# Performance work log

Hardware: AMD Instinct MI355X
Metric: run time of the kernel (lower is better)

The kernel has to match this reference:

```python
import jax, jax.numpy as jnp
import numpy as np

NUM_LEVELS = 16
BASE_RES = 16
MAX_RES = 2048
F_PER_LEVEL = 2
MAX_TABLE = 524288  # 2**19
N_POINTS = 1048576
# geometric resolution schedule, identical to the torch module
RESOLUTIONS = [int(BASE_RES * (MAX_RES / BASE_RES) ** (l / (NUM_LEVELS - 1))) for l in range(NUM_LEVELS)]
TABLE_SIZES = [min(r ** 3, MAX_TABLE) for r in RESOLUTIONS]


def setup_inputs() -> dict:
    key = jax.random.key(0)
    k0, k1, k2, k3 = jax.random.split(key, 4)
    coords = jax.random.uniform(k0, (N_POINTS, 3), minval=-1.0, maxval=1.0, dtype=jnp.float32)
    # hash tables init U(-1e-4, 1e-4); all padded to MAX_TABLE rows (levels with
    # smaller dense tables simply never index past TABLE_SIZES[l])
    tables = jax.random.uniform(k1, (NUM_LEVELS, MAX_TABLE, F_PER_LEVEL), minval=-1e-4, maxval=1e-4, dtype=jnp.float32)
    d_in = NUM_LEVELS * F_PER_LEVEL  # 32
    W1 = jax.random.normal(k2, (d_in, 128), dtype=jnp.float32) * (2.0 / (d_in + 128)) ** 0.5
    b1 = jnp.zeros((128,), dtype=jnp.float32)
    W2 = jax.random.normal(k3, (128, 64), dtype=jnp.float32) * (2.0 / (128 + 64)) ** 0.5
    b2 = jnp.zeros((64,), dtype=jnp.float32)
    return {"coords": coords, "tables": tables, "W1": W1, "b1": b1, "W2": W2, "b2": b2}


def _hash_gather(coords, tables):
    # coords: [N, 3] in [-1, 1] -> normalized to [0, 1]
    c = (coords + 1.0) * 0.5
    feats = []
    for l in range(NUM_LEVELS):
        R = RESOLUTIONS[l]
        T = TABLE_SIZES[l]
        d = jnp.clip(jnp.floor(c * R).astype(jnp.int32), 0, R - 1).astype(jnp.uint32)  # [N, 3]
        # (x*R^2 + y*R + z) % T in uint32. Wraparound mod 2^32 only occurs at the
        # finest levels where T = 2^19 divides 2^32, so the result stays exact.
        idx = (d[:, 0] * jnp.uint32(R * R) + d[:, 1] * jnp.uint32(R) + d[:, 2]) % jnp.uint32(T)
        feats.append(tables[l][idx.astype(jnp.int32)])  # [N, F_PER_LEVEL]
    return jnp.concatenate(feats, axis=-1)  # [N, 32], level-major


def reference(coords, tables, W1, b1, W2, b2):
    x = _hash_gather(coords, tables)              # [N, 32]
    h = jax.nn.relu(x @ W1 + b1)                  # [N, 128]
    return h @ W2 + b2                            # [N, 64]
```

## Files before the change

### kernel.cpp

```cpp
#include <hip/hip_runtime.h>
#include <stdint.h>


typedef __attribute__((ext_vector_type(8))) __bf16 bf16x8;
typedef __attribute__((ext_vector_type(4))) float  f32x4;
typedef __attribute__((ext_vector_type(2))) float  f32x2;

#define NPTS   1048576
#define NTILES 65536

__device__ const unsigned kRES[16] = {16u,22u,30u,42u,58u,80u,111u,153u,
                                      212u,294u,406u,561u,776u,1072u,1482u,2048u};

__device__ __forceinline__ unsigned pack_bf16(float x, float y) {
  __bf16 a = (__bf16)x, b = (__bf16)y;
  unsigned short ua, ub;
  __builtin_memcpy(&ua, &a, 2);
  __builtin_memcpy(&ub, &b, 2);
  return (unsigned)ua | ((unsigned)ub << 16);
}

__global__ __launch_bounds__(256) void tconv_prep_kernel(
    const float* __restrict__ tables,
    const float* __restrict__ W1, const float* __restrict__ W2,
    unsigned* __restrict__ tb2, short* __restrict__ w1p, short* __restrict__ w2p)
{
  if (blockIdx.x < 8192) {
    int e0 = (blockIdx.x * 256 + threadIdx.x) * 4;
#pragma unroll
    for (int i = 0; i < 4; ++i) {
      int e = e0 + i;
      f32x2 f = *(const f32x2*)(tables + (size_t)e * 2);
      tb2[e] = pack_bf16(f.x, f.y);
    }
    return;
  }
  int tid = (blockIdx.x - 8192) * 256 + threadIdx.x;
  int l = tid & 63;
  int g = l >> 4;
  int c = l & 15;
  if (tid < 512) {
    int t = tid >> 6;
    bf16x8 v;
#pragma unroll
    for (int j = 0; j < 8; ++j)
      v[j] = (__bf16)W1[(8*g + j)*128 + 16*t + c];
    *(bf16x8*)(w1p + (size_t)(t*64 + l)*8) = v;
  } else if (tid < 1536) {
    int e = (tid - 512) >> 6;
    int mt = e >> 2, ks = e & 3;
    bf16x8 v;
#pragma unroll
    for (int j = 0; j < 8; ++j)
      v[j] = (__bf16)W2[(32*ks + 16*(j>>2) + 4*g + (j&3))*64 + 16*mt + c];
    *(bf16x8*)(w2p + (size_t)(e*64 + l)*8) = v;
  }
}

__global__ __launch_bounds__(256) void gather_kernel(
    const float* __restrict__ coords, const unsigned* __restrict__ tb2,
    unsigned* __restrict__ xw)
{
  const int xcd = blockIdx.x & 7;
  const int j   = blockIdx.x >> 3;
  int lv, chunk;
  if (j < 1408) {
    int ghi = xcd * 1408 + j;
    lv = 5 + (ghi >> 10);
    chunk = ghi & 1023;
  } else {
    int gei = xcd * 640 + (j - 1408);
    lv = gei >> 10;
    chunk = gei & 1023;
  }

  const unsigned R = kRES[lv];
  const float fR = (float)R;
  const unsigned RR = R * R;
  const unsigned Rm1 = R - 1u;
  const unsigned M = (lv >= 6) ? 0x7FFFFu : 0xFFFFFFFFu;
  const unsigned* tb = tb2 + ((size_t)lv << 19);
  unsigned* xp = xw + ((size_t)lv << 20);

  int p0 = chunk * 1024 + threadIdx.x;
#pragma unroll
  for (int i = 0; i < 4; ++i) {
    int p = p0 + (i << 8);
    float u0 = (coords[3*p+0] + 1.0f) * 0.5f;
    float u1 = (coords[3*p+1] + 1.0f) * 0.5f;
    float u2 = (coords[3*p+2] + 1.0f) * 0.5f;
    unsigned d0 = (unsigned)(int)(u0 * fR); if (d0 > Rm1) d0 = Rm1;
    unsigned d1 = (unsigned)(int)(u1 * fR); if (d1 > Rm1) d1 = Rm1;
    unsigned d2 = (unsigned)(int)(u2 * fR); if (d2 > Rm1) d2 = Rm1;
    unsigned idx = (d0*RR + d1*R + d2) & M;
    xp[p] = tb[idx];
  }
}

__global__ __launch_bounds__(256, 4) void mlp_kernel(
    const unsigned* __restrict__ xw,
    const float* __restrict__ b1, const float* __restrict__ b2,
    const short* __restrict__ w1p, const short* __restrict__ w2p,
    float* __restrict__ out)
{
  const int l = threadIdx.x & 63;
  const int g = l >> 4;
  const int c = l & 15;
  const int w = threadIdx.x >> 6;

  __shared__ float obuf[4][16][68];

  bf16x8 w1f[8];
#pragma unroll
  for (int t = 0; t < 8; ++t)
    w1f[t] = *(const bf16x8*)(w1p + (size_t)(t*64 + l)*8);

  const int base = blockIdx.x * 4 + w;

  unsigned gx[4][4];
#pragma unroll
  for (int it = 0; it < 4; ++it) {
    int p = (base + it*16384)*16 + c;
#pragma unroll
    for (int q = 0; q < 4; ++q)
      gx[it][q] = xw[((size_t)(4*g + q) << 20) + p];
  }

#pragma unroll
  for (int it = 0; it < 4; ++it) {
    union { bf16x8 v; unsigned u[4]; } X;
#pragma unroll
    for (int q = 0; q < 4; ++q) X.u[q] = gx[it][q];
    bf16x8 xf = X.v;

    f32x4 h[8];
#pragma unroll
    for (int t = 0; t < 8; ++t) {
      h[t] = *(const f32x4*)(b1 + 16*t + 4*g);
      h[t] = __builtin_amdgcn_mfma_f32_16x16x32_bf16(w1f[t], xf, h[t], 0, 0, 0);
    }

    f32x4 o[4];
#pragma unroll
    for (int mt = 0; mt < 4; ++mt)
      o[mt] = *(const f32x4*)(b2 + 16*mt + 4*g);
#pragma unroll
    for (int ks = 0; ks < 4; ++ks) {
      bf16x8 bp;
#pragma unroll
      for (int j = 0; j < 8; ++j) {
        float v = h[2*ks + (j>>2)][j & 3];
        v = fmaxf(v, 0.0f);
        bp[j] = (__bf16)v;
      }
#pragma unroll
      for (int mt = 0; mt < 4; ++mt) {
        bf16x8 w2f = *(const bf16x8*)(w2p + (size_t)((mt*4 + ks)*64 + l)*8);
        o[mt] = __builtin_amdgcn_mfma_f32_16x16x32_bf16(w2f, bp, o[mt], 0, 0, 0);
      }
    }

    float (*ob)[68] = obuf[w];
#pragma unroll
    for (int mt = 0; mt < 4; ++mt)
      *(f32x4*)&ob[c][16*mt + 4*g] = o[mt];
    asm volatile("s_waitcnt lgkmcnt(0)" ::: "memory");
    f32x4 v[4];
#pragma unroll
    for (int s = 0; s < 4; ++s)
      v[s] = *(const f32x4*)&ob[4*s + g][4*c];
    asm volatile("" ::: "memory");
    float* op = out + (size_t)(base + it*16384) * 1024;
#pragma unroll
    for (int s = 0; s < 4; ++s)
      *(f32x4*)(op + (4*s + g)*64 + 4*c) = v[s];

    if (it < 3) asm volatile("s_waitcnt lgkmcnt(0)" ::: "memory");
  }
}

__global__ void prep_kernel(const float* __restrict__ W1, const float* __restrict__ W2,
                            short* __restrict__ w1p, short* __restrict__ w2p) {
  int tid = blockIdx.x * blockDim.x + threadIdx.x;
  int l = tid & 63;
  int g = l >> 4;
  int c = l & 15;
  if (tid < 512) {
    int t = tid >> 6;
    bf16x8 v;
#pragma unroll
    for (int j = 0; j < 8; ++j)
      v[j] = (__bf16)W1[(8*g + j)*128 + 16*t + c];
    *(bf16x8*)(w1p + (size_t)(t*64 + l)*8) = v;
  } else if (tid < 1536) {
    int e = (tid - 512) >> 6;
    int mt = e >> 2, ks = e & 3;
    bf16x8 v;
#pragma unroll
    for (int j = 0; j < 8; ++j)
      v[j] = (__bf16)W2[(32*ks + 16*(j>>2) + 4*g + (j&3))*64 + 16*mt + c];
    *(bf16x8*)(w2p + (size_t)(e*64 + l)*8) = v;
  }
}

__global__ __launch_bounds__(256, 3) void hashgrid_mlp_kernel(
    const float* __restrict__ coords, const float* __restrict__ tables,
    const float* __restrict__ b1, const float* __restrict__ b2,
    const short* __restrict__ w1p, const short* __restrict__ w2p,
    float* __restrict__ out, int stride)
{
  const int l = threadIdx.x & 63;
  const int g = l >> 4;
  const int c = l & 15;

  unsigned Rq[4], RRq[4], Mq[4]; float fRq[4];
#pragma unroll
  for (int q = 0; q < 4; ++q) {
    int lv = 4*g + q;
    unsigned R = kRES[lv];
    Rq[q] = R; RRq[q] = R*R; fRq[q] = (float)R;
    Mq[q] = (lv >= 6) ? 0x7FFFFu : 0xFFFFFFFFu;
  }
  const float* tb = tables + ((size_t)g << 22);

  bf16x8 w1f[8];
#pragma unroll
  for (int t = 0; t < 8; ++t)
    w1f[t] = *(const bf16x8*)(w1p + (size_t)(t*64 + l)*8);

  f32x2 gx[4];
  auto prefetch = [&](int tile) {
    int p = tile*16 + c;
    float u0 = (coords[3*p+0] + 1.0f) * 0.5f;
    float u1 = (coords[3*p+1] + 1.0f) * 0.5f;
    float u2 = (coords[3*p+2] + 1.0f) * 0.5f;
#pragma unroll
    for (int q = 0; q < 4; ++q) {
      unsigned Rm1 = Rq[q] - 1u;
      unsigned d0 = (unsigned)(int)(u0 * fRq[q]); if (d0 > Rm1) d0 = Rm1;
      unsigned d1 = (unsigned)(int)(u1 * fRq[q]); if (d1 > Rm1) d1 = Rm1;
      unsigned d2 = (unsigned)(int)(u2 * fRq[q]); if (d2 > Rm1) d2 = Rm1;
      unsigned idx = (d0*RRq[q] + d1*Rq[q] + d2) & Mq[q];
      gx[q] = *(const f32x2*)(tb + ((size_t)q << 20) + (size_t)idx*2u);
    }
  };

  int tile = blockIdx.x * 4 + (threadIdx.x >> 6);
  prefetch(tile);
  while (true) {
    bf16x8 xf;
#pragma unroll
    for (int q = 0; q < 4; ++q) {
      xf[2*q]   = (__bf16)gx[q].x;
      xf[2*q+1] = (__bf16)gx[q].y;
    }
    int cur = tile;
    tile += stride;
    if (tile < NTILES) prefetch(tile);

    f32x4 h[8];
#pragma unroll
    for (int t = 0; t < 8; ++t) {
      h[t] = *(const f32x4*)(b1 + 16*t + 4*g);
      h[t] = __builtin_amdgcn_mfma_f32_16x16x32_bf16(w1f[t], xf, h[t], 0, 0, 0);
    }

    f32x4 o[4];
#pragma unroll
    for (int mt = 0; mt < 4; ++mt)
      o[mt] = *(const f32x4*)(b2 + 16*mt + 4*g);
#pragma unroll
    for (int ks = 0; ks < 4; ++ks) {
      bf16x8 bp;
#pragma unroll
      for (int j = 0; j < 8; ++j) {
        float v = h[2*ks + (j>>2)][j & 3];
        v = fmaxf(v, 0.0f);
        bp[j] = (__bf16)v;
      }
#pragma unroll
      for (int mt = 0; mt < 4; ++mt) {
        bf16x8 w2f = *(const bf16x8*)(w2p + (size_t)((mt*4 + ks)*64 + l)*8);
        o[mt] = __builtin_amdgcn_mfma_f32_16x16x32_bf16(w2f, bp, o[mt], 0, 0, 0);
      }
    }

    float* op = out + (size_t)(cur*16 + c)*64 + 4*g;
#pragma unroll
    for (int mt = 0; mt < 4; ++mt)
      *(f32x4*)(op + 16*mt) = o[mt];

    if (tile >= NTILES) break;
  }
}

extern "C" void kernel_launch(void* const* d_in, const int* in_sizes, int n_in,
                              void* d_out, int out_size, void* d_ws, size_t ws_size,
                              hipStream_t stream) {
  const float* coords = (const float*)d_in[0];
  const float* tables = (const float*)d_in[1];
  const float* W1     = (const float*)d_in[2];
  const float* b1     = (const float*)d_in[3];
  const float* W2     = (const float*)d_in[4];
  const float* b2     = (const float*)d_in[5];
  float* out = (float*)d_out;

  short* w1p = (short*)d_ws;
  short* w2p = w1p + 4096;

  const size_t XW_OFF  = 32*1024;
  const size_t XW_SZ   = (size_t)NPTS * 16 * 4;
  const size_t TB2_SZ  = (size_t)16 * 524288 * 4;
  const size_t need = XW_OFF + XW_SZ + TB2_SZ;

  if (ws_size >= need) {
    unsigned* xw  = (unsigned*)((char*)d_ws + XW_OFF);
    unsigned* tb2 = (unsigned*)((char*)d_ws + XW_OFF + XW_SZ);
    tconv_prep_kernel<<<8198, 256, 0, stream>>>(tables, W1, W2, tb2, w1p, w2p);
    gather_kernel<<<16384, 256, 0, stream>>>(coords, tb2, xw);
    mlp_kernel<<<4096, 256, 0, stream>>>(xw, b1, b2, w1p, w2p, out);
  } else {
    prep_kernel<<<6, 256, 0, stream>>>(W1, W2, w1p, w2p);
    const int blocks = 2048;
    hashgrid_mlp_kernel<<<blocks, 256, 0, stream>>>(coords, tables, b1, b2,
                                                    w1p, w2p, out, blocks*4);
  }
}
```

Measured before the change: 188.3 us.

## Fuse hash gather and MLP into one kernel with LDS transpose

Replaces the separate gather kernel, which wrote a 64 MB bf16 feature buffer to global memory, and the MLP kernel that read it back, with one fused kernel. Each thread computes all 16 level indices for one point, gathers the packed table entries into registers, and stages them in shared memory so the MFMA fragments can be read per 16-point tile. This removes the intermediate global write and read plus one launch. The cost is that the level-interleaved, XCD-aware gather schedule is lost, so the random table accesses from all 16 levels now compete for L2 at the same time, and the kernel uses more registers and LDS.

```diff
diff --git a/kernel.cpp b/kernel.cpp
--- a/kernel.cpp
+++ b/kernel.cpp
@@ -8,9 +8,6 @@
 
 #define NPTS   1048576
 #define NTILES 65536
-
-__device__ const unsigned kRES[16] = {16u,22u,30u,42u,58u,80u,111u,153u,
-                                      212u,294u,406u,561u,776u,1072u,1482u,2048u};
 
 __device__ __forceinline__ unsigned pack_bf16(float x, float y) {
   __bf16 a = (__bf16)x, b = (__bf16)y;
@@ -57,48 +54,8 @@
   }
 }
 
-__global__ __launch_bounds__(256) void gather_kernel(
+__global__ __launch_bounds__(256) void fused_kernel(
     const float* __restrict__ coords, const unsigned* __restrict__ tb2,
-    unsigned* __restrict__ xw)
-{
-  const int xcd = blockIdx.x & 7;
-  const int j   = blockIdx.x >> 3;
-  int lv, chunk;
-  if (j < 1408) {
-    int ghi = xcd * 1408 + j;
-    lv = 5 + (ghi >> 10);
-    chunk = ghi & 1023;
-  } else {
-    int gei = xcd * 640 + (j - 1408);
-    lv = gei >> 10;
-    chunk = gei & 1023;
-  }
-
-  const unsigned R = kRES[lv];
-  const float fR = (float)R;
-  const unsigned RR = R * R;
-  const unsigned Rm1 = R - 1u;
-  const unsigned M = (lv >= 6) ? 0x7FFFFu : 0xFFFFFFFFu;
-  const unsigned* tb = tb2 + ((size_t)lv << 19);
-  unsigned* xp = xw + ((size_t)lv << 20);
-
-  int p0 = chunk * 1024 + threadIdx.x;
-#pragma unroll
-  for (int i = 0; i < 4; ++i) {
-    int p = p0 + (i << 8);
-    float u0 = (coords[3*p+0] + 1.0f) * 0.5f;
-    float u1 = (coords[3*p+1] + 1.0f) * 0.5f;
-    float u2 = (coords[3*p+2] + 1.0f) * 0.5f;
-    unsigned d0 = (unsigned)(int)(u0 * fR); if (d0 > Rm1) d0 = Rm1;
-    unsigned d1 = (unsigned)(int)(u1 * fR); if (d1 > Rm1) d1 = Rm1;
-    unsigned d2 = (unsigned)(int)(u2 * fR); if (d2 > Rm1) d2 = Rm1;
-    unsigned idx = (d0*RR + d1*R + d2) & M;
-    xp[p] = tb[idx];
-  }
-}
-
-__global__ __launch_bounds__(256, 4) void mlp_kernel(
-    const unsigned* __restrict__ xw,
     const float* __restrict__ b1, const float* __restrict__ b2,
     const short* __restrict__ w1p, const short* __restrict__ w2p,
     float* __restrict__ out)
@@ -108,36 +65,56 @@
   const int c = l & 15;
   const int w = threadIdx.x >> 6;
 
+  __shared__ unsigned xbuf[256][20];
   __shared__ float obuf[4][16][68];
+
+  constexpr unsigned Rt[16] = {16u,22u,30u,42u,58u,80u,111u,153u,
+                               212u,294u,406u,561u,776u,1072u,1482u,2048u};
 
   bf16x8 w1f[8];
 #pragma unroll
   for (int t = 0; t < 8; ++t)
     w1f[t] = *(const bf16x8*)(w1p + (size_t)(t*64 + l)*8);
 
-  const int base = blockIdx.x * 4 + w;
-
-  unsigned gx[4][4];
-#pragma unroll
-  for (int it = 0; it < 4; ++it) {
-    int p = (base + it*16384)*16 + c;
-#pragma unroll
-    for (int q = 0; q < 4; ++q)
-      gx[it][q] = xw[((size_t)(4*g + q) << 20) + p];
-  }
-
-#pragma unroll
-  for (int it = 0; it < 4; ++it) {
-    union { bf16x8 v; unsigned u[4]; } X;
-#pragma unroll
-    for (int q = 0; q < 4; ++q) X.u[q] = gx[it][q];
+  const int ptl = w*64 + l;
+  const int p   = blockIdx.x*256 + ptl;
+  const float u0 = (coords[3*p+0] + 1.0f) * 0.5f;
+  const float u1 = (coords[3*p+1] + 1.0f) * 0.5f;
+  const float u2 = (coords[3*p+2] + 1.0f) * 0.5f;
+
+  unsigned idx[16];
+#pragma unroll
+  for (int lv = 0; lv < 16; ++lv) {
+    const unsigned R = Rt[lv];
+    const float fR = (float)R;
+    const unsigned Rm1 = R - 1u;
+    const unsigned M = (lv >= 6) ? 0x7FFFFu : 0xFFFFFFFFu;
+    unsigned d0 = (unsigned)(int)(u0 * fR); if (d0 > Rm1) d0 = Rm1;
+    unsigned d1 = (unsigned)(int)(u1 * fR); if (d1 > Rm1) d1 = Rm1;
+    unsigned d2 = (unsigned)(int)(u2 * fR); if (d2 > Rm1) d2 = Rm1;
+    idx[lv] = (d0*(R*R) + d1*R + d2) & M;
+  }
+  unsigned val[16];
+#pragma unroll
+  for (int lv = 0; lv < 16; ++lv)
+    val[lv] = tb2[((size_t)lv << 19) + idx[lv]];
+#pragma unroll
+  for (int lv = 0; lv < 16; ++lv)
+    xbuf[ptl][lv] = val[lv];
+  asm volatile("s_waitcnt lgkmcnt(0)" ::: "memory");
+  __builtin_amdgcn_sched_barrier(0);
+
+#pragma unroll
+  for (int t = 0; t < 4; ++t) {
+    union { bf16x8 v; f32x4 f; } X;
+    X.f = *(const f32x4*)&xbuf[w*64 + t*16 + c][4*g];
     bf16x8 xf = X.v;
 
     f32x4 h[8];
 #pragma unroll
-    for (int t = 0; t < 8; ++t) {
-      h[t] = *(const f32x4*)(b1 + 16*t + 4*g);
-      h[t] = __builtin_amdgcn_mfma_f32_16x16x32_bf16(w1f[t], xf, h[t], 0, 0, 0);
+    for (int tt = 0; tt < 8; ++tt) {
+      h[tt] = *(const f32x4*)(b1 + 16*tt + 4*g);
+      h[tt] = __builtin_amdgcn_mfma_f32_16x16x32_bf16(w1f[tt], xf, h[tt], 0, 0, 0);
     }
 
     f32x4 o[4];
@@ -170,12 +147,11 @@
     for (int s = 0; s < 4; ++s)
       v[s] = *(const f32x4*)&ob[4*s + g][4*c];
     asm volatile("" ::: "memory");
-    float* op = out + (size_t)(base + it*16384) * 1024;
+    float* op = out + (size_t)(blockIdx.x*16 + w*4 + t) * 1024;
 #pragma unroll
     for (int s = 0; s < 4; ++s)
       *(f32x4*)(op + (4*s + g)*64 + 4*c) = v[s];
-
-    if (it < 3) asm volatile("s_waitcnt lgkmcnt(0)" ::: "memory");
+    if (t < 3) asm volatile("s_waitcnt lgkmcnt(0)" ::: "memory");
   }
 }
 
@@ -202,6 +178,9 @@
     *(bf16x8*)(w2p + (size_t)(e*64 + l)*8) = v;
   }
 }
+
+__device__ const unsigned kRES[16] = {16u,22u,30u,42u,58u,80u,111u,153u,
+                                      212u,294u,406u,561u,776u,1072u,1482u,2048u};
 
 __global__ __launch_bounds__(256, 3) void hashgrid_mlp_kernel(
     const float* __restrict__ coords, const float* __restrict__ tables,
@@ -308,17 +287,14 @@
   short* w1p = (short*)d_ws;
   short* w2p = w1p + 4096;
 
-  const size_t XW_OFF  = 32*1024;
-  const size_t XW_SZ   = (size_t)NPTS * 16 * 4;
+  const size_t TB2_OFF = 32*1024;
   const size_t TB2_SZ  = (size_t)16 * 524288 * 4;
-  const size_t need = XW_OFF + XW_SZ + TB2_SZ;
+  const size_t need = TB2_OFF + TB2_SZ;
 
   if (ws_size >= need) {
-    unsigned* xw  = (unsigned*)((char*)d_ws + XW_OFF);
-    unsigned* tb2 = (unsigned*)((char*)d_ws + XW_OFF + XW_SZ);
+    unsigned* tb2 = (unsigned*)((char*)d_ws + TB2_OFF);
     tconv_prep_kernel<<<8198, 256, 0, stream>>>(tables, W1, W2, tb2, w1p, w2p);
-    gather_kernel<<<16384, 256, 0, stream>>>(coords, tb2, xw);
-    mlp_kernel<<<4096, 256, 0, stream>>>(xw, b1, b2, w1p, w2p, out);
+    fused_kernel<<<4096, 256, 0, stream>>>(coords, tb2, b1, b2, w1p, w2p, out);
   } else {
     prep_kernel<<<6, 256, 0, stream>>>(W1, W2, w1p, w2p);
     const int blocks = 2048;
```

Result: slower. 287.6 us (+52.7%).

## Fuse coarse hash levels into one gather pass and halve MLP per-block work

Applied to the files above, without the earlier changes.

The gather kernel's blocks for the five coarse levels (0-4) now process all five levels for each point, so coordinates are read once instead of five times. This cuts the gather grid from 16384 to 12288 blocks, and the resolution table becomes a compile-time constant. The MLP kernel now handles two tiles per wave instead of four and launches twice as many blocks, trading register prefetch depth for more parallelism. Coarse-level blocks do more serial work, which may unbalance the load against the fine-level blocks.

```diff
diff --git a/kernel.cpp b/kernel.cpp
--- a/kernel.cpp
+++ b/kernel.cpp
@@ -8,9 +8,6 @@
 
 #define NPTS   1048576
 #define NTILES 65536
-
-__device__ const unsigned kRES[16] = {16u,22u,30u,42u,58u,80u,111u,153u,
-                                      212u,294u,406u,561u,776u,1072u,1482u,2048u};
 
 __device__ __forceinline__ unsigned pack_bf16(float x, float y) {
   __bf16 a = (__bf16)x, b = (__bf16)y;
@@ -61,39 +58,57 @@
     const float* __restrict__ coords, const unsigned* __restrict__ tb2,
     unsigned* __restrict__ xw)
 {
+  constexpr unsigned Rt[16] = {16u,22u,30u,42u,58u,80u,111u,153u,
+                               212u,294u,406u,561u,776u,1072u,1482u,2048u};
   const int xcd = blockIdx.x & 7;
   const int j   = blockIdx.x >> 3;
-  int lv, chunk;
+
   if (j < 1408) {
     int ghi = xcd * 1408 + j;
-    lv = 5 + (ghi >> 10);
-    chunk = ghi & 1023;
+    int lv = 5 + (ghi >> 10);
+    int chunk = ghi & 1023;
+
+    const unsigned R = Rt[lv];
+    const float fR = (float)R;
+    const unsigned RR = R * R;
+    const unsigned Rm1 = R - 1u;
+    const unsigned M = (lv >= 6) ? 0x7FFFFu : 0xFFFFFFFFu;
+    const unsigned* tb = tb2 + ((size_t)lv << 19);
+    unsigned* xp = xw + ((size_t)lv << 20);
+
+    int p0 = chunk * 1024 + threadIdx.x;
+#pragma unroll
+    for (int i = 0; i < 4; ++i) {
+      int p = p0 + (i << 8);
+      float u0 = (coords[3*p+0] + 1.0f) * 0.5f;
+      float u1 = (coords[3*p+1] + 1.0f) * 0.5f;
+      float u2 = (coords[3*p+2] + 1.0f) * 0.5f;
+      unsigned d0 = (unsigned)(int)(u0 * fR); if (d0 > Rm1) d0 = Rm1;
+      unsigned d1 = (unsigned)(int)(u1 * fR); if (d1 > Rm1) d1 = Rm1;
+      unsigned d2 = (unsigned)(int)(u2 * fR); if (d2 > Rm1) d2 = Rm1;
+      unsigned idx = (d0*RR + d1*R + d2) & M;
+      xp[p] = tb[idx];
+    }
   } else {
-    int gei = xcd * 640 + (j - 1408);
-    lv = gei >> 10;
-    chunk = gei & 1023;
-  }
-
-  const unsigned R = kRES[lv];
-  const float fR = (float)R;
-  const unsigned RR = R * R;
-  const unsigned Rm1 = R - 1u;
-  const unsigned M = (lv >= 6) ? 0x7FFFFu : 0xFFFFFFFFu;
-  const unsigned* tb = tb2 + ((size_t)lv << 19);
-  unsigned* xp = xw + ((size_t)lv << 20);
-
-  int p0 = chunk * 1024 + threadIdx.x;
-#pragma unroll
-  for (int i = 0; i < 4; ++i) {
-    int p = p0 + (i << 8);
-    float u0 = (coords[3*p+0] + 1.0f) * 0.5f;
-    float u1 = (coords[3*p+1] + 1.0f) * 0.5f;
-    float u2 = (coords[3*p+2] + 1.0f) * 0.5f;
-    unsigned d0 = (unsigned)(int)(u0 * fR); if (d0 > Rm1) d0 = Rm1;
-    unsigned d1 = (unsigned)(int)(u1 * fR); if (d1 > Rm1) d1 = Rm1;
-    unsigned d2 = (unsigned)(int)(u2 * fR); if (d2 > Rm1) d2 = Rm1;
-    unsigned idx = (d0*RR + d1*R + d2) & M;
-    xp[p] = tb[idx];
+    int chunk = xcd * 128 + (j - 1408);
+    int p0 = chunk * 1024 + threadIdx.x;
+#pragma unroll
+    for (int i = 0; i < 4; ++i) {
+      int p = p0 + (i << 8);
+      float u0 = (coords[3*p+0] + 1.0f) * 0.5f;
+      float u1 = (coords[3*p+1] + 1.0f) * 0.5f;
+      float u2 = (coords[3*p+2] + 1.0f) * 0.5f;
+#pragma unroll
+      for (int lv = 0; lv < 5; ++lv) {
+        const unsigned R = Rt[lv];
+        const unsigned Rm1 = R - 1u;
+        unsigned d0 = (unsigned)(int)(u0 * (float)R); if (d0 > Rm1) d0 = Rm1;
+        unsigned d1 = (unsigned)(int)(u1 * (float)R); if (d1 > Rm1) d1 = Rm1;
+        unsigned d2 = (unsigned)(int)(u2 * (float)R); if (d2 > Rm1) d2 = Rm1;
+        unsigned idx = d0*(R*R) + d1*R + d2;
+        xw[((size_t)lv << 20) + p] = tb2[((size_t)lv << 19) + idx];
+      }
+    }
   }
 }
 
@@ -117,17 +132,17 @@
 
   const int base = blockIdx.x * 4 + w;
 
-  unsigned gx[4][4];
-#pragma unroll
-  for (int it = 0; it < 4; ++it) {
-    int p = (base + it*16384)*16 + c;
+  unsigned gx[2][4];
+#pragma unroll
+  for (int it = 0; it < 2; ++it) {
+    int p = (base + it*32768)*16 + c;
 #pragma unroll
     for (int q = 0; q < 4; ++q)
       gx[it][q] = xw[((size_t)(4*g + q) << 20) + p];
   }
 
 #pragma unroll
-  for (int it = 0; it < 4; ++it) {
+  for (int it = 0; it < 2; ++it) {
     union { bf16x8 v; unsigned u[4]; } X;
 #pragma unroll
     for (int q = 0; q < 4; ++q) X.u[q] = gx[it][q];
@@ -170,12 +185,12 @@
     for (int s = 0; s < 4; ++s)
       v[s] = *(const f32x4*)&ob[4*s + g][4*c];
     asm volatile("" ::: "memory");
-    float* op = out + (size_t)(base + it*16384) * 1024;
+    float* op = out + (size_t)(base + it*32768) * 1024;
 #pragma unroll
     for (int s = 0; s < 4; ++s)
       *(f32x4*)(op + (4*s + g)*64 + 4*c) = v[s];
 
-    if (it < 3) asm volatile("s_waitcnt lgkmcnt(0)" ::: "memory");
+    if (it < 1) asm volatile("s_waitcnt lgkmcnt(0)" ::: "memory");
   }
 }
 
@@ -202,6 +217,9 @@
     *(bf16x8*)(w2p + (size_t)(e*64 + l)*8) = v;
   }
 }
+
+__device__ const unsigned kRES[16] = {16u,22u,30u,42u,58u,80u,111u,153u,
+                                      212u,294u,406u,561u,776u,1072u,1482u,2048u};
 
 __global__ __launch_bounds__(256, 3) void hashgrid_mlp_kernel(
     const float* __restrict__ coords, const float* __restrict__ tables,
@@ -317,8 +335,8 @@
     unsigned* xw  = (unsigned*)((char*)d_ws + XW_OFF);
     unsigned* tb2 = (unsigned*)((char*)d_ws + XW_OFF + XW_SZ);
     tconv_prep_kernel<<<8198, 256, 0, stream>>>(tables, W1, W2, tb2, w1p, w2p);
-    gather_kernel<<<16384, 256, 0, stream>>>(coords, tb2, xw);
-    mlp_kernel<<<4096, 256, 0, stream>>>(xw, b1, b2, w1p, w2p, out);
+    gather_kernel<<<12288, 256, 0, stream>>>(coords, tb2, xw);
+    mlp_kernel<<<8192, 256, 0, stream>>>(xw, b1, b2, w1p, w2p, out);
   } else {
     prep_kernel<<<6, 256, 0, stream>>>(W1, W2, w1p, w2p);
     const int blocks = 2048;
```

Measured after the change: 188.3 us. No clear change (+0.0%).
